# Kernel tuning notes

Hardware: AMD Instinct MI355X
Metric: run time of the kernel (lower is better)

Reference implementation:

```python
import jax, jax.numpy as jnp
import numpy as np

H = 16
D_K = 64
HALF_WINDOW = 256  # window_size // 2 = 512 // 2


def setup_inputs() -> dict:
    key = jax.random.key(0)
    ks = jax.random.split(key, 9)
    B, S, D = 2, 2048, 1024
    scale = 0.02
    return {
        "x": jax.random.normal(ks[0], (B, S, D), dtype=jnp.float32),
        "Wq": jax.random.normal(ks[1], (D, D), dtype=jnp.float32) * scale,
        "bq": jax.random.normal(ks[2], (D,), dtype=jnp.float32) * scale,
        "Wk": jax.random.normal(ks[3], (D, D), dtype=jnp.float32) * scale,
        "bk": jax.random.normal(ks[4], (D,), dtype=jnp.float32) * scale,
        "Wv": jax.random.normal(ks[5], (D, D), dtype=jnp.float32) * scale,
        "bv": jax.random.normal(ks[6], (D,), dtype=jnp.float32) * scale,
        "Wo": jax.random.normal(ks[7], (D, D), dtype=jnp.float32) * scale,
        "bo": jax.random.normal(ks[8], (D,), dtype=jnp.float32) * scale,
    }


def reference(x, Wq, bq, Wk, bk, Wv, bv, Wo, bo):
    B, S, D = x.shape
    # projections -> [B, H, S, d_k]
    q = (x @ Wq + bq).reshape(B, S, H, D_K).transpose(0, 2, 1, 3)
    k = (x @ Wk + bk).reshape(B, S, H, D_K).transpose(0, 2, 1, 3)
    v = (x @ Wv + bv).reshape(B, S, H, D_K).transpose(0, 2, 1, 3)
    # dense scores, as in the original module
    scores = jnp.einsum("bhqd,bhkd->bhqk", q, k) / jnp.sqrt(jnp.float32(D_K))
    # sliding window band mask: 0 inside |i-j| <= half_window, -inf outside
    idx = jnp.arange(S)
    band = jnp.abs(idx[:, None] - idx[None, :]) <= HALF_WINDOW  # [S, S]
    window_mask = jnp.where(band, jnp.float32(0.0), -jnp.inf)
    scores = scores + window_mask[None, None, :, :]
    attn = jax.nn.softmax(scores, axis=-1)  # dropout is identity (p=0 / eval)
    out = jnp.einsum("bhqk,bhkd->bhqd", attn, v)  # [B, H, S, d_k]
    out = out.transpose(0, 2, 1, 3).reshape(B, S, D)
    return out @ Wo + bo
```

## Files before the change

### kernel.cpp

```cpp
#include <hip/hip_runtime.h>
#include <hip/hip_bf16.h>
#include <cstdint>
#include <cstddef>

using bf16 = __hip_bfloat16;
typedef __attribute__((ext_vector_type(8))) short bf16x8v;
typedef __attribute__((ext_vector_type(4))) float f32x4v;
typedef __attribute__((ext_vector_type(16))) float f32x16v;
typedef __attribute__((ext_vector_type(4))) int i32x4v;

__device__ __forceinline__ f32x4v mfma16x16x32(bf16x8v a, bf16x8v b, f32x4v c) {
  return __builtin_amdgcn_mfma_f32_16x16x32_bf16(a, b, c, 0, 0, 0);
}
__device__ __forceinline__ f32x16v mfma32x32x16(bf16x8v a, bf16x8v b, f32x16v c) {
  return __builtin_amdgcn_mfma_f32_32x32x16_bf16(a, b, c, 0, 0, 0);
}

__device__ __forceinline__ void lds_async16(const void* g, void* l) {
  __builtin_amdgcn_global_load_lds(
      (__attribute__((address_space(1))) void*)g,
      (__attribute__((address_space(3))) void*)l, 16, 0, 0);
}

__device__ __forceinline__ unsigned short f2bf_bits(float f) {
  union { bf16 h; unsigned short u; } cv;
  cv.h = __float2bfloat16(f);
  return cv.u;
}
__device__ __forceinline__ uint32_t pk_bf2(float a, float b) {
  return (uint32_t)f2bf_bits(a) | ((uint32_t)f2bf_bits(b) << 16);
}

#define QSC 0.18033688011111793f

__global__ void prep_k(const float* __restrict__ x,
                       const float* __restrict__ Wq, const float* __restrict__ Wk,
                       const float* __restrict__ Wv, const float* __restrict__ Wo,
                       const float* __restrict__ bq, const float* __restrict__ bk,
                       const float* __restrict__ bv,
                       bf16* __restrict__ xb, bf16* __restrict__ wcat,
                       bf16* __restrict__ wot, float* __restrict__ bcat)
{
  __shared__ float tile[64][65];
  const int bid = blockIdx.x;
  if (bid < 4096) {
    const int i = bid * 256 + threadIdx.x;
    const float4 v = reinterpret_cast<const float4*>(x)[i];
    ushort4 o;
    o.x = f2bf_bits(v.x); o.y = f2bf_bits(v.y);
    o.z = f2bf_bits(v.z); o.w = f2bf_bits(v.w);
    reinterpret_cast<ushort4*>(xb)[i] = o;
  } else if (bid < 5120) {
    const int b2 = bid - 4096;
    const int mat = b2 >> 8;
    const float* W = (mat == 0) ? Wq : (mat == 1) ? Wk : (mat == 2) ? Wv : Wo;
    bf16* dst = (mat < 3) ? (wcat + (size_t)mat * 1024 * 1024) : wot;
    const int n0 = ((b2 >> 4) & 15) * 64, k0 = (b2 & 15) * 64;
    const int tr = threadIdx.x >> 6, tc = threadIdx.x & 63;
#pragma unroll
    for (int it = 0; it < 16; ++it)
      tile[it * 4 + tr][tc] = W[(size_t)(k0 + it * 4 + tr) * 1024 + n0 + tc];
    __syncthreads();
#pragma unroll
    for (int it = 0; it < 16; ++it) {
      const int n = n0 + it * 4 + tr;
      dst[(size_t)n * 1024 + k0 + tc] = __float2bfloat16(tile[tc][it * 4 + tr]);
    }
  } else {
    const int i = (bid - 5120) * 256 + threadIdx.x;
    if (i < 3072)
      bcat[i] = (i < 1024) ? bq[i] : (i < 2048) ? bk[i - 1024] : bv[i - 2048];
  }
}

template <int EPI>
__global__ __launch_bounds__(256, 3) void gemm_k(
    const bf16* __restrict__ A, const bf16* __restrict__ Bt,
    const float* __restrict__ bias,
    bf16* __restrict__ qb, bf16* __restrict__ kb, bf16* __restrict__ vtb,
    float* __restrict__ outf)
{
  constexpr int K = 1024;
  __shared__ bf16 smem[16384];
  const int t = threadIdx.x;
  const int lane = t & 63, w = t >> 6;
  const int g = lane >> 4, r = lane & 15;
  const int wr = w >> 1, wc = w & 1;
  const int m0 = blockIdx.x * 128, n0 = blockIdx.y * 128;

  const int srow = t >> 2;
  const int scol = ((lane & 3) ^ g) << 3;
  const bf16* aS0 = A + (size_t)(m0 + srow) * K + scol;
  const bf16* aS1 = A + (size_t)(m0 + 64 + srow) * K + scol;
  const bf16* bS0 = Bt + (size_t)(n0 + srow) * K + scol;
  const bf16* bS1 = Bt + (size_t)(n0 + 64 + srow) * K + scol;

  f32x4v acc[4][4] = {};

  auto STAGE = [&](int kt, int buf) {
    const int ko = kt * 32;
    char* d0 = (char*)smem + buf * 16384 + w * 1024;
    lds_async16(aS0 + ko, d0);
    lds_async16(aS1 + ko, d0 + 4096);
    lds_async16(bS0 + ko, d0 + 8192);
    lds_async16(bS1 + ko, d0 + 12288);
  };

  const int csw = (g ^ ((r >> 2) & 3)) << 4;

  STAGE(0, 0);
  asm volatile("s_waitcnt vmcnt(0)" ::: "memory");
  __builtin_amdgcn_s_barrier();

  for (int kt = 0; kt < 32; ++kt) {
    if (kt < 31) STAGE(kt + 1, (kt + 1) & 1);

    const char* buf = (const char*)smem + (kt & 1) * 16384;
    bf16x8v af[4], bfr[4];
#pragma unroll
    for (int m = 0; m < 4; ++m)
      af[m] = *reinterpret_cast<const bf16x8v*>(buf + (wr * 64 + m * 16 + r) * 64 + csw);
#pragma unroll
    for (int n = 0; n < 4; ++n)
      bfr[n] = *reinterpret_cast<const bf16x8v*>(buf + 8192 + (wc * 64 + n * 16 + r) * 64 + csw);
#pragma unroll
    for (int m = 0; m < 4; ++m)
#pragma unroll
      for (int n = 0; n < 4; ++n)
        acc[m][n] = mfma16x16x32(af[m], bfr[n], acc[m][n]);

    if (kt < 31) asm volatile("s_waitcnt vmcnt(0)" ::: "memory");
    __builtin_amdgcn_s_barrier();
  }

  if (EPI == 0) {
    const int gcol0 = n0 + wc * 64;
    const int mat = gcol0 >> 10;
    const int hh = (gcol0 & 1023) >> 6;
    const int s0 = m0 + wr * 64;
    const int b_ = s0 >> 11, sb = s0 & 2047;
    const size_t bh = (size_t)(b_ * 16 + hh);
    unsigned short* ep = (unsigned short*)smem + w * 4096;

#pragma unroll
    for (int n = 0; n < 4; ++n) {
      const int dkl = n * 16 + r;
      const float bv_ = bias[gcol0 + dkl];
#pragma unroll
      for (int m = 0; m < 4; ++m) {
#pragma unroll
        for (int v = 0; v < 4; ++v) {
          const int sl = m * 16 + g * 4 + v;
          const float val = acc[m][n][v] + bv_;
          if (mat == 0)      ep[sl * 64 + dkl] = f2bf_bits(val * QSC);
          else if (mat == 1) ep[sl * 64 + dkl] = f2bf_bits(val);
          else               ep[dkl * 64 + sl] = f2bf_bits(val);
        }
      }
    }
#pragma unroll
    for (int i = 0; i < 8; ++i) {
      const int chunk = i * 64 + lane;
      const int rw = chunk >> 3;
      const int off = (chunk & 7) * 8;
      const bf16x8v vv = *reinterpret_cast<const bf16x8v*>(ep + rw * 64 + off);
      if (mat == 0)
        *reinterpret_cast<bf16x8v*>(qb + (bh * 2048 + sb + rw) * 64 + off) = vv;
      else if (mat == 1)
        *reinterpret_cast<bf16x8v*>(kb + (bh * 2048 + sb + rw) * 64 + off) = vv;
      else
        *reinterpret_cast<bf16x8v*>(vtb + (bh * 64 + rw) * 2048 + sb + off) = vv;
    }
  } else {
#pragma unroll
    for (int n = 0; n < 4; ++n) {
      const int gcol = n0 + wc * 64 + n * 16 + r;
      const float bv_ = bias[gcol];
#pragma unroll
      for (int m = 0; m < 4; ++m) {
#pragma unroll
        for (int v = 0; v < 4; ++v) {
          const int grow = m0 + wr * 64 + m * 16 + g * 4 + v;
          outf[(size_t)grow * 1024 + gcol] = acc[m][n][v] + bv_;
        }
      }
    }
  }
}

__global__ __launch_bounds__(128) void attn_k(
    const bf16* __restrict__ qb, const bf16* __restrict__ kb_,
    const bf16* __restrict__ vtb, bf16* __restrict__ aout)
{
  constexpr int S = 2048;
  const int tid = threadIdx.x;
  const int wid = tid >> 6;
  const int lane = tid & 63;
  const int hi = lane >> 5, l31 = lane & 31;
  const int d_ = blockIdx.x;
  const int xcd = d_ & 7, slot = d_ >> 3;
  const int bh_i = xcd * 4 + (slot >> 6);
  const int q0 = (slot & 63) * 32;
  const int b = bh_i >> 4, h = bh_i & 15;
  const size_t bh = (size_t)b * 16 + h;
  const bf16* qp = qb + bh * (size_t)(S * 64);
  const bf16* kp = kb_ + bh * (size_t)(S * 64);
  const bf16* vp = vtb + bh * (size_t)(64 * S);

  __shared__ float msum[64 * 33];

  bf16x8v qf[4];
#pragma unroll
  for (int i = 0; i < 4; ++i)
    qf[i] = *reinterpret_cast<const bf16x8v*>(&qp[(size_t)(q0 + l31) * 64 + i * 16 + hi * 8]);

  f32x16v o0 = {}, o1 = {};
  float lrun = 0.f;

  const int jlo = (q0 >= 256) ? (q0 - 256) : 0;
  const int jend = (q0 + 256 <= S - 32) ? (q0 + 256) : (S - 32);
  const int nIter = ((jend - jlo) >> 5) + 1;
  const int h_ = (nIter + 1) >> 1;
  const int myN = wid ? (nIter - h_) : h_;
  const int jlo_w = jlo + (wid ? h_ * 32 : 0);

  auto LDK = [&](int j, bf16x8v* kf) {
    const bf16* p0 = kp + (size_t)(j + l31) * 64 + hi * 8;
#pragma unroll
    for (int i = 0; i < 4; ++i)
      kf[i] = *reinterpret_cast<const bf16x8v*>(p0 + i * 16);
  };
  auto LDV = [&](int j, bf16x8v* vf) {
#pragma unroll
    for (int db = 0; db < 2; ++db)
#pragma unroll
      for (int kk = 0; kk < 2; ++kk)
        vf[db * 2 + kk] = *reinterpret_cast<const bf16x8v*>(
            &vp[(size_t)(db * 32 + l31) * S + j + kk * 16 + hi * 8]);
  };

  auto STEP = [&](int idx, bf16x8v* kc, bf16x8v* vc, bf16x8v* kn, bf16x8v* vn) {
    const int j = jlo_w + idx * 32;
    if (idx + 1 < myN) { LDK(j + 32, kn); LDV(j + 32, vn); }

    f32x16v s = {};
#pragma unroll
    for (int i = 0; i < 4; ++i) s = mfma32x32x16(kc[i], qf[i], s);

    float p[16];
    const bool needMask = ((q0 + 31 - j) > 256) || ((j + 31 - q0) > 256);
    if (needMask) {
      const int base = l31 - 4 * hi + (q0 - j) + 256;
#pragma unroll
      for (int tt = 0; tt < 4; ++tt)
#pragma unroll
        for (int e = 0; e < 4; ++e) {
          const int kk_ = 8 * tt + e;
          const float ev = __builtin_amdgcn_exp2f(s[4 * tt + e]);
          p[4 * tt + e] = ((unsigned)(base - kk_) <= 512u) ? ev : 0.f;
        }
    } else {
#pragma unroll
      for (int i = 0; i < 16; ++i) p[i] = __builtin_amdgcn_exp2f(s[i]);
    }
    lrun += (((p[0] + p[1]) + (p[2] + p[3])) + ((p[4] + p[5]) + (p[6] + p[7]))) +
            (((p[8] + p[9]) + (p[10] + p[11])) + ((p[12] + p[13]) + (p[14] + p[15])));

    uint32_t W00 = pk_bf2(p[0],  p[1]),  W01 = pk_bf2(p[2],  p[3]);
    uint32_t W10 = pk_bf2(p[4],  p[5]),  W11 = pk_bf2(p[6],  p[7]);
    uint32_t W20 = pk_bf2(p[8],  p[9]),  W21 = pk_bf2(p[10], p[11]);
    uint32_t W30 = pk_bf2(p[12], p[13]), W31 = pk_bf2(p[14], p[15]);
    asm volatile("v_permlane32_swap_b32 %0, %1" : "+v"(W00), "+v"(W10));
    asm volatile("v_permlane32_swap_b32 %0, %1" : "+v"(W01), "+v"(W11));
    asm volatile("v_permlane32_swap_b32 %0, %1" : "+v"(W20), "+v"(W30));
    asm volatile("v_permlane32_swap_b32 %0, %1" : "+v"(W21), "+v"(W31));
    union { i32x4v i; bf16x8v hv; } c0, c1;
    c0.i = (i32x4v){(int)W00, (int)W01, (int)W10, (int)W11};
    c1.i = (i32x4v){(int)W20, (int)W21, (int)W30, (int)W31};
    o0 = mfma32x32x16(vc[0], c0.hv, o0);
    o0 = mfma32x32x16(vc[1], c1.hv, o0);
    o1 = mfma32x32x16(vc[2], c0.hv, o1);
    o1 = mfma32x32x16(vc[3], c1.hv, o1);
  };

  bf16x8v ka[4], va[4], kn2[4], vn2[4];
  LDK(jlo_w, ka); LDV(jlo_w, va);
  int it = 0;
  while (it + 2 <= myN) {
    STEP(it, ka, va, kn2, vn2);
    STEP(it + 1, kn2, vn2, ka, va);
    it += 2;
  }
  if (it < myN) STEP(it, ka, va, kn2, vn2);

  if (wid == 1) {
    float* mp = msum + lane * 33;
#pragma unroll
    for (int i = 0; i < 16; ++i) { mp[i] = o0[i]; mp[16 + i] = o1[i]; }
    mp[32] = lrun;
  }
  __syncthreads();
  if (wid == 0) {
    const float* mp = msum + lane * 33;
#pragma unroll
    for (int i = 0; i < 16; ++i) { o0[i] += mp[i]; o1[i] += mp[16 + i]; }
    lrun += mp[32];
    lrun += __shfl_xor(lrun, 32);
    const float inv = 1.0f / lrun;

    const size_t ob = ((size_t)b * S + q0 + l31) * 1024 + h * 64 + hi * 4;
#pragma unroll
    for (int tt = 0; tt < 4; ++tt) {
      uint2 u;
      u.x = pk_bf2(o0[4 * tt] * inv, o0[4 * tt + 1] * inv);
      u.y = pk_bf2(o0[4 * tt + 2] * inv, o0[4 * tt + 3] * inv);
      *reinterpret_cast<uint2*>(&aout[ob + 8 * tt]) = u;
      uint2 v2;
      v2.x = pk_bf2(o1[4 * tt] * inv, o1[4 * tt + 1] * inv);
      v2.y = pk_bf2(o1[4 * tt + 2] * inv, o1[4 * tt + 3] * inv);
      *reinterpret_cast<uint2*>(&aout[ob + 32 + 8 * tt]) = v2;
    }
  }
}

extern "C" void kernel_launch(void* const* d_in, const int* in_sizes, int n_in,
                              void* d_out, int out_size, void* d_ws, size_t ws_size,
                              hipStream_t stream) {
  (void)in_sizes; (void)n_in; (void)out_size; (void)ws_size;
  const float* x  = (const float*)d_in[0];
  const float* Wq = (const float*)d_in[1];
  const float* bq = (const float*)d_in[2];
  const float* Wk = (const float*)d_in[3];
  const float* bk = (const float*)d_in[4];
  const float* Wv = (const float*)d_in[5];
  const float* bv = (const float*)d_in[6];
  const float* Wo = (const float*)d_in[7];
  const float* bo = (const float*)d_in[8];
  float* out = (float*)d_out;

  char* ws = (char*)d_ws;
  bf16*  xb    = (bf16*)(ws);
  bf16*  wcat  = (bf16*)(ws + 8388608);
  bf16*  wot   = (bf16*)(ws + 14680064);
  bf16*  qbuf  = (bf16*)(ws + 16777216);
  bf16*  kbuf  = (bf16*)(ws + 25165824);
  bf16*  vtbuf = (bf16*)(ws + 33554432);
  bf16*  aoutb = (bf16*)(ws + 41943040);
  float* bcat  = (float*)(ws + 50331648);

  prep_k<<<5132, 256, 0, stream>>>(x, Wq, Wk, Wv, Wo, bq, bk, bv,
                                   xb, wcat, wot, bcat);

  gemm_k<0><<<dim3(32, 24), 256, 0, stream>>>(xb, wcat, bcat, qbuf, kbuf, vtbuf, nullptr);
  attn_k<<<2048, 128, 0, stream>>>(qbuf, kbuf, vtbuf, aoutb);
  gemm_k<1><<<dim3(32, 8), 256, 0, stream>>>(aoutb, wot, bo, nullptr, nullptr, nullptr, out);
}
```

Measured before the change: 102.0 us.

## Split attention key range across four waves and vectorize weight transpose stores

The attention kernel now launches 256 threads per block and splits each query tile's key-block range across four waves instead of two, merging the partial outputs and row sums through a larger shared buffer. This shortens each wave's serial chain of MFMA and exp work per block and adds parallelism, at the cost of more shared-memory reduction traffic and more per-block overhead. Separately, the weight-transpose prep path now writes four bf16 values per thread as one ushort4 store instead of scalar stores, to cut store instruction count.

Measured after the change: 104.1 us. 2.1% more time.

```diff
diff --git a/kernel.cpp b/kernel.cpp
--- a/kernel.cpp
+++ b/kernel.cpp
@@ -62,9 +62,15 @@
       tile[it * 4 + tr][tc] = W[(size_t)(k0 + it * 4 + tr) * 1024 + n0 + tc];
     __syncthreads();
 #pragma unroll
-    for (int it = 0; it < 16; ++it) {
-      const int n = n0 + it * 4 + tr;
-      dst[(size_t)n * 1024 + k0 + tc] = __float2bfloat16(tile[tc][it * 4 + tr]);
+    for (int i = 0; i < 4; ++i) {
+      const int idx = i * 256 + threadIdx.x;
+      const int n = idx >> 4, c = idx & 15;
+      ushort4 o;
+      o.x = f2bf_bits(tile[4 * c + 0][n]);
+      o.y = f2bf_bits(tile[4 * c + 1][n]);
+      o.z = f2bf_bits(tile[4 * c + 2][n]);
+      o.w = f2bf_bits(tile[4 * c + 3][n]);
+      *reinterpret_cast<ushort4*>(dst + (size_t)(n0 + n) * 1024 + k0 + 4 * c) = o;
     }
   } else {
     const int i = (bid - 5120) * 256 + threadIdx.x;
@@ -188,7 +194,7 @@
   }
 }
 
-__global__ __launch_bounds__(128) void attn_k(
+__global__ __launch_bounds__(256) void attn_k(
     const bf16* __restrict__ qb, const bf16* __restrict__ kb_,
     const bf16* __restrict__ vtb, bf16* __restrict__ aout)
 {
@@ -207,7 +213,7 @@
   const bf16* kp = kb_ + bh * (size_t)(S * 64);
   const bf16* vp = vtb + bh * (size_t)(64 * S);
 
-  __shared__ float msum[64 * 33];
+  __shared__ float msum[3][64][33];
 
   bf16x8v qf[4];
 #pragma unroll
@@ -220,9 +226,9 @@
   const int jlo = (q0 >= 256) ? (q0 - 256) : 0;
   const int jend = (q0 + 256 <= S - 32) ? (q0 + 256) : (S - 32);
   const int nIter = ((jend - jlo) >> 5) + 1;
-  const int h_ = (nIter + 1) >> 1;
-  const int myN = wid ? (nIter - h_) : h_;
-  const int jlo_w = jlo + (wid ? h_ * 32 : 0);
+  const int base_ = nIter >> 2, rem = nIter & 3;
+  const int myN = base_ + (wid < rem ? 1 : 0);
+  const int jlo_w = jlo + 32 * (wid * base_ + (wid < rem ? wid : rem));
 
   auto LDK = [&](int j, bf16x8v* kf) {
     const bf16* p0 = kp + (size_t)(j + l31) * 64 + hi * 8;
@@ -250,14 +256,14 @@
     float p[16];
     const bool needMask = ((q0 + 31 - j) > 256) || ((j + 31 - q0) > 256);
     if (needMask) {
-      const int base = l31 - 4 * hi + (q0 - j) + 256;
+      const int base2 = l31 - 4 * hi + (q0 - j) + 256;
 #pragma unroll
       for (int tt = 0; tt < 4; ++tt)
 #pragma unroll
         for (int e = 0; e < 4; ++e) {
           const int kk_ = 8 * tt + e;
           const float ev = __builtin_amdgcn_exp2f(s[4 * tt + e]);
-          p[4 * tt + e] = ((unsigned)(base - kk_) <= 512u) ? ev : 0.f;
+          p[4 * tt + e] = ((unsigned)(base2 - kk_) <= 512u) ? ev : 0.f;
         }
     } else {
 #pragma unroll
@@ -293,18 +299,21 @@
   }
   if (it < myN) STEP(it, ka, va, kn2, vn2);
 
-  if (wid == 1) {
-    float* mp = msum + lane * 33;
+  if (wid != 0) {
+    float* mp = &msum[wid - 1][lane][0];
 #pragma unroll
     for (int i = 0; i < 16; ++i) { mp[i] = o0[i]; mp[16 + i] = o1[i]; }
     mp[32] = lrun;
   }
   __syncthreads();
   if (wid == 0) {
-    const float* mp = msum + lane * 33;
-#pragma unroll
-    for (int i = 0; i < 16; ++i) { o0[i] += mp[i]; o1[i] += mp[16 + i]; }
-    lrun += mp[32];
+#pragma unroll
+    for (int wv = 0; wv < 3; ++wv) {
+      const float* mp = &msum[wv][lane][0];
+#pragma unroll
+      for (int i = 0; i < 16; ++i) { o0[i] += mp[i]; o1[i] += mp[16 + i]; }
+      lrun += mp[32];
+    }
     lrun += __shfl_xor(lrun, 32);
     const float inv = 1.0f / lrun;
 
@@ -352,6 +361,6 @@
                                    xb, wcat, wot, bcat);
 
   gemm_k<0><<<dim3(32, 24), 256, 0, stream>>>(xb, wcat, bcat, qbuf, kbuf, vtbuf, nullptr);
-  attn_k<<<2048, 128, 0, stream>>>(qbuf, kbuf, vtbuf, aoutb);
+  attn_k<<<2048, 256, 0, stream>>>(qbuf, kbuf, vtbuf, aoutb);
   gemm_k<1><<<dim3(32, 8), 256, 0, stream>>>(aoutb, wot, bo, nullptr, nullptr, nullptr, out);
 }
```
